# Kernel optimization log

Hardware: AMD Instinct MI355X
Metric: run time of the kernel (lower is better)

The kernel has to match this reference:

```python
import jax, jax.numpy as jnp
import numpy as np

D, H, W = 40, 32, 88
BEV_H, BEV_W = 125, 125
X_MIN, X_MAX, DX = -50.0, 50.0, 0.8
Y_MIN, Y_MAX, DY = -50.0, 50.0, 0.8
Z_MIN, DZ = -10.0, 20.0


def _voxel_indices():
    """Replicates frustum creation + get_geometry + index computation.
    Returns (flat_idx, valid) each of shape (D, H, W). Faithful to the
    original's sequential in-place max() semantics."""
    # depth_grid = arange(1, 41, 1) + 1  -> 2..41
    depth = jnp.arange(1.0, 41.0, 1.0) + 1.0            # (D,)
    xs = jnp.linspace(0.0, W - 1.0, W)                  # (W,)
    ys = jnp.linspace(0.0, H - 1.0, H)                  # (H,)
    d = depth[:, None, None]                            # (D,1,1)
    xd = jnp.broadcast_to(xs[None, None, :] * d, (D, H, W))  # x*depth
    yd = jnp.broadcast_to(ys[None, :, None] * d, (D, H, W))  # y*depth
    zd = jnp.broadcast_to(d, (D, H, W))                       # depth
    # first points_d.max(): over columns (xd, yd, zd)
    max1 = jnp.maximum(xd.max(), jnp.maximum(yd.max(), zd.max()))
    gx = xd / max1 * (X_MAX - X_MIN) + X_MIN
    # second points_d.max(): column 0 was overwritten in-place by gx
    max2 = jnp.maximum(gx.max(), jnp.maximum(yd.max(), zd.max()))
    gy = yd / max2 * (Y_MAX - Y_MIN) + Y_MIN
    gz = zd
    # voxelize (torch .long() truncates; all values here are >= 0)
    ix = ((gx - X_MIN) / DX).astype(jnp.int32)
    iy = ((gy - Y_MIN) / DY).astype(jnp.int32)
    iz = ((gz - Z_MIN) / DZ).astype(jnp.int32)
    valid = (ix >= 0) & (ix < BEV_W) & (iy >= 0) & (iy < BEV_H) & (iz >= 0)
    flat_idx = jnp.where(valid, iy * BEV_W + ix, 0)
    return flat_idx, valid


def setup_inputs() -> dict:
    key = jax.random.key(0)
    k1, k2, k3, k4, k5 = jax.random.split(key, 5)
    B, N, C = 1, 6, 128
    return {
        "img_feat": jax.random.normal(k1, (B, N, C, H, W), dtype=jnp.float32),
        "depth_logits": jax.random.normal(k2, (B, N, D, H, W), dtype=jnp.float32),
        "rots": jax.random.normal(k3, (B, N, 3, 3), dtype=jnp.float32),
        "trans": jax.random.normal(k4, (B, N, 3), dtype=jnp.float32),
        "intrins": jax.random.normal(k5, (B, N, 3, 3), dtype=jnp.float32),
    }


def reference(img_feat, depth_logits, rots, trans, intrins):
    B, N, C, h, w = img_feat.shape
    depth_probs = jax.nn.softmax(depth_logits, axis=2)         # (B,N,D,H,W)
    # depth-weighted outer product: (B,N,D,H,W,C)
    feats = jnp.einsum('bnchw,bndhw->bndhwc', img_feat, depth_probs)
    flat_feats = feats.reshape(-1, C)                          # (B*N*D*H*W, C)
    flat_idx, valid = _voxel_indices()                         # (D,H,W)
    idx = jnp.broadcast_to(flat_idx[None, None], (B, N, D, h, w)).reshape(-1)
    msk = jnp.broadcast_to(valid[None, None], (B, N, D, h, w)).reshape(-1)
    flat_feats = jnp.where(msk[:, None], flat_feats, 0.0)
    bev = jax.ops.segment_sum(flat_feats, idx, num_segments=BEV_H * BEV_W)
    bev = bev.reshape(BEV_H, BEV_W, C)
    return jnp.transpose(bev, (2, 0, 1))[None]                 # (1, C, 125, 125)
```

## Files before the change

kernel.cpp:

```cpp
#include <hip/hip_runtime.h>


constexpr int D = 40, H = 32, W = 88, HW = H * W;
constexpr int C = 128, NCAM = 6;
constexpr int BEV = 125, NBINS = BEV * BEV;
constexpr int NCOLS = NCAM * HW;
constexpr int LISTCAP = 192;

typedef __attribute__((ext_vector_type(8))) unsigned short us8;
typedef __attribute__((ext_vector_type(4))) float f4;

__device__ __forceinline__ unsigned short f2bf(float x) {
    unsigned u = __float_as_uint(x);
    return (unsigned short)((u + 0x7FFF + ((u >> 16) & 1)) >> 16);
}
__device__ __forceinline__ float b2f(unsigned short u) {
    return __uint_as_float(((unsigned)u) << 16);
}

struct Tabs { short XP[D][126]; short YP[D][126]; };
constexpr Tabs make_tabs() {
    Tabs t{};
    for (int d = 0; d < D; ++d) {
        int dep = d + 2;
        int cntx[126] = {};
        for (int w = 0; w < W; ++w) {
            float gx = (float)(w * dep) / 3567.0f * 100.0f - 50.0f;
            int ix = (int)((gx + 50.0f) / 0.8f);
            if (ix < 125) cntx[ix]++;
        }
        t.XP[d][0] = 0;
        for (int X = 0; X < 125; ++X) t.XP[d][X + 1] = (short)(t.XP[d][X] + cntx[X]);
        int cnty[126] = {};
        for (int h = 0; h < H; ++h) {
            float gy = (float)(h * dep) / 1271.0f * 100.0f - 50.0f;
            int iy = (int)((gy + 50.0f) / 0.8f);
            if (iy < 125) cnty[iy]++;
        }
        t.YP[d][0] = 0;
        for (int Y = 0; Y < 125; ++Y) t.YP[d][Y + 1] = (short)(t.YP[d][Y] + cnty[Y]);
    }
    return t;
}
__device__ const Tabs g_tab = make_tabs();

struct SegTable { unsigned a[4096]; unsigned b[4096]; int n; };

constexpr SegTable make_segs() {
    SegTable S{};
    Tabs t = make_tabs();
    int ns = 0;
    for (int iy = 0; iy < 125; ++iy) {
        int cnt[125] = {};
        for (int d = 0; d < D; ++d) {
            int yc = t.YP[d][iy + 1] - t.YP[d][iy];
            if (yc == 0) continue;
            for (int X = 0; X < 125; ++X)
                cnt[X] += (t.XP[d][X + 1] - t.XP[d][X]) * yc;
        }
        int X = 0;
        while (X < 125) {
            if (cnt[X] > 176) {
                int d0 = 0;
                while (d0 < D) {
                    int run = 0, d1 = d0;
                    while (d1 < D) {
                        int piece = (t.XP[d1][X + 1] - t.XP[d1][X]) *
                                    (t.YP[d1][iy + 1] - t.YP[d1][iy]);
                        if (d1 > d0 && run + piece > 128) break;
                        run += piece; ++d1;
                    }
                    if (run > 0) {
                        S.a[ns] = ((unsigned)iy << 16) | ((unsigned)X << 8) | (unsigned)(X + 1);
                        S.b[ns] = (1u << 31) | ((unsigned)d0 << 25) | ((unsigned)d1 << 19) | (unsigned)run;
                        ++ns;
                    }
                    d0 = d1;
                }
                ++X;
            } else {
                int X0 = X, run = 0;
                while (X < 125 && (X - X0) < 16 && cnt[X] <= 176 &&
                       (X == X0 || run + cnt[X] <= 128)) {
                    run += cnt[X]; ++X;
                }
                if (run > 0) {
                    S.a[ns] = ((unsigned)iy << 16) | ((unsigned)X0 << 8) | (unsigned)X;
                    S.b[ns] = ((unsigned)0 << 25) | ((unsigned)D << 19) | (unsigned)run;
                    ++ns;
                }
            }
        }
    }
    S.n = ns;
    return S;
}
constexpr SegTable g_raw = make_segs();

constexpr SegTable reorder_segs() {
    SegTable R{};
    int pos = 0;
    for (int i = 0; i < g_raw.n; ++i)
        if ((int)(g_raw.b[i] & 0x7FFFF) >= 120) { R.a[pos] = g_raw.a[i]; R.b[pos] = g_raw.b[i]; ++pos; }
    for (int i = 0; i < g_raw.n; ++i)
        if ((int)(g_raw.b[i] & 0x7FFFF) <  120) { R.a[pos] = g_raw.a[i]; R.b[pos] = g_raw.b[i]; ++pos; }
    R.n = pos;
    return R;
}
constexpr SegTable g_ct = reorder_segs();
constexpr int NSEG = g_ct.n;
static_assert(NSEG > 0 && NSEG <= 4096, "seg table overflow");
__device__ const SegTable g_segs = g_ct;

constexpr int PACK_BLOCKS = (C / 8) * (HW / 32);
constexpr int SMAX_BLOCKS = NCOLS / 256;
constexpr int ZERO_TOTAL  = C * NBINS / 4;
constexpr int ZERO_BLOCKS = (ZERO_TOTAL + 1023) / 1024;
constexpr int MEGA_BLOCKS = PACK_BLOCKS + SMAX_BLOCKS + ZERO_BLOCKS;

__global__ void __launch_bounds__(256) mega_kernel(
        const float* __restrict__ feat,
        const float* __restrict__ logits,
        float* __restrict__ probs_t,
        unsigned short* __restrict__ feat_p,
        float* __restrict__ out) {
    __shared__ __align__(16) float tile[NCAM * 8 * 37];
    int b = blockIdx.x, t = threadIdx.x;

    if (b < PACK_BLOCKS) {
        int c0  = (b / 88) * 8;
        int hw0 = (b % 88) * 32;
        int cq = t >> 5, hwL = t & 31;
#pragma unroll
        for (int n = 0; n < NCAM; ++n)
            tile[(n * 8 + cq) * 37 + hwL] =
                feat[((size_t)(n * C + c0 + cq)) * HW + hw0 + hwL];
        __syncthreads();
        int hl = t >> 3, cL = t & 7;
        us8 v;
#pragma unroll
        for (int n = 0; n < NCAM; ++n)
            v[n] = f2bf(tile[(n * 8 + cL) * 37 + hl]);
        v[6] = 0; v[7] = 0;
        *(us8*)(feat_p + ((size_t)(hw0 + hl) * C + (c0 + cL)) * 8) = v;

    } else if (b < PACK_BLOCKS + SMAX_BLOCKS) {
        int col = (b - PACK_BLOCKS) * 256 + t;
        int n  = col / HW;
        int hw = col - n * HW;
        const float* src = logits + ((size_t)n * D) * HW + hw;
        float v[D];
        float m = -3.402823466e+38f;
#pragma unroll
        for (int d = 0; d < D; ++d) {
            v[d] = src[(size_t)d * HW];
            m = fmaxf(m, v[d]);
        }
        float s = 0.f;
#pragma unroll
        for (int d = 0; d < D; ++d) { v[d] = expf(v[d] - m); s += v[d]; }
        float inv = 1.0f / s;
#pragma unroll
        for (int d = 0; d < D; ++d)
            probs_t[(size_t)((d << 12) | hw) * 8 + n] = v[d] * inv;

    } else {
        int base = (b - PACK_BLOCKS - SMAX_BLOCKS) * 1024;
#pragma unroll
        for (int k = 0; k < 4; ++k) {
            int i = base + k * 256 + t;
            if (i < ZERO_TOTAL) ((f4*)out)[i] = f4{0.f, 0.f, 0.f, 0.f};
        }
    }
}

__global__ void __launch_bounds__(128, 4) gather_kernel(
        const unsigned short* __restrict__ feat_p,
        const float* __restrict__ probs_t,
        float* __restrict__ out) {
    __shared__ float T[2][16][66];
    __shared__ unsigned list[LISTCAP];
    int slot  = blockIdx.x >> 1;
    int chalf = blockIdx.x & 1;
    unsigned da = g_segs.a[slot], db = g_segs.b[slot];
    int iy = da >> 16, X0 = (da >> 8) & 0xFF, X1 = da & 0xFF;
    int width = X1 - X0;
    bool split = (db >> 31) != 0;
    int d0 = (db >> 25) & 0x3F, d1 = (db >> 19) & 0x3F;
    int P  = (int)(db & 0x7FFFF);
    int t = threadIdx.x;

    if (t < 64) {
        int d = d0 + t;
        if (d < d1) {
            int off = 0;
            for (int dd = d0; dd < d; ++dd)
                off += (g_tab.YP[dd][iy + 1] - g_tab.YP[dd][iy]) *
                       (g_tab.XP[dd][X1] - g_tab.XP[dd][X0]);
            int hb = g_tab.YP[d][iy], he = g_tab.YP[d][iy + 1];
            int p = off;
            for (int bl = 0; bl < width; ++bl) {
                int wb = g_tab.XP[d][X0 + bl], we = g_tab.XP[d][X0 + bl + 1];
                for (int h = hb; h < he; ++h)
                    for (int w = wb; w < we; ++w)
                        list[p++] = ((unsigned)bl << 18) | ((unsigned)d << 12)
                                  | (unsigned)(h * W + w);
            }
        }
    } else {
        float* Tf = &T[0][0][0];
        for (int i = t - 64; i < 2 * 16 * 66; i += 64) Tf[i] = 0.f;
    }
    __syncthreads();

    int lane = t & 63, dg = t >> 6;
    int c = chalf * 64 + lane;
    float* Tp = &T[dg][0][0];

    int npts = (P - dg + 1) >> 1;
    float racc = 0.f;
    int rbl = -1;

#define FETCH(I, BUF, P_)                                                     \
    { pk##BUF[I] = (unsigned)__shfl(myent, (P_));                             \
      fv##BUF[I] = *(const us8*)(feat_p +                                     \
                    (((size_t)(pk##BUF[I] & 0xFFFu) * C + (unsigned)c) * 8)); \
      const float* pp_ = probs_t + ((size_t)(pk##BUF[I] & 0x3FFFFu) << 3);    \
      pa##BUF[I] = *(const f4*)pp_; pb##BUF[I] = *(const f4*)(pp_ + 4); }
#define CONSUME(I, BUF)                                                       \
    { float s_ = pa##BUF[I].x * b2f(fv##BUF[I][0]) + pa##BUF[I].y * b2f(fv##BUF[I][1]) \
               + pa##BUF[I].z * b2f(fv##BUF[I][2]) + pa##BUF[I].w * b2f(fv##BUF[I][3]) \
               + pb##BUF[I].x * b2f(fv##BUF[I][4]) + pb##BUF[I].y * b2f(fv##BUF[I][5]);\
      int bl_ = (int)(pk##BUF[I] >> 18);                                      \
      if (bl_ != rbl) { if (rbl >= 0) Tp[rbl * 66 + lane] += racc;            \
                        rbl = bl_; racc = s_; }                               \
      else racc += s_; }

    int li0 = min(dg + 2 * lane, LISTCAP - 1);
    int myent_next = (int)list[li0];
    for (int kb = 0; kb < npts; kb += 64) {
        int myent = myent_next;
        if (kb + 64 < npts) {
            int li = min(dg + 2 * (kb + 64 + lane), LISTCAP - 1);
            myent_next = (int)list[li];
        }
        int win = min(64, npts - kb);
        unsigned pkA[3], pkB[3]; us8 fvA[3], fvB[3];
        f4 paA[3], pbA[3], paB[3], pbB[3];
#pragma unroll
        for (int i = 0; i < 3; ++i) if (i < win) FETCH(i, A, i);
        for (int j = 0; j < win; j += 6) {
#pragma unroll
            for (int i = 0; i < 3; ++i) { int p = j + 3 + i;
                if (p < win) FETCH(i, B, p); }
#pragma unroll
            for (int i = 0; i < 3; ++i) { int p = j + i;
                if (p < win) CONSUME(i, A); }
#pragma unroll
            for (int i = 0; i < 3; ++i) { int p = j + 6 + i;
                if (p < win) FETCH(i, A, p); }
#pragma unroll
            for (int i = 0; i < 3; ++i) { int p = j + 3 + i;
                if (p < win) CONSUME(i, B); }
        }
    }
    if (rbl >= 0) Tp[rbl * 66 + lane] += racc;
    __syncthreads();
#undef FETCH
#undef CONSUME

    int binbase = iy * BEV + X0;
#pragma unroll
    for (int it = 0; it < 8; ++it) {
        int bl = t & 15, cc = it * 8 + (t >> 4);
        if (bl < width) {
            float v = T[0][bl][cc] + T[1][bl][cc];
            float* dst = &out[(size_t)(chalf * 64 + cc) * NBINS + binbase + bl];
            if (split) atomicAdd(dst, v);
            else       *dst = v;
        }
    }
}

extern "C" void kernel_launch(void* const* d_in, const int* in_sizes, int n_in,
                              void* d_out, int out_size, void* d_ws, size_t ws_size,
                              hipStream_t stream) {
    const float* img_feat     = (const float*)d_in[0];
    const float* depth_logits = (const float*)d_in[1];
    float* out = (float*)d_out;

    char* p = (char*)d_ws;
    float*          probs_t = (float*)p;          p += (size_t)D * 4096 * 8 * 4;
    unsigned short* feat_p  = (unsigned short*)p; p += (size_t)HW * C * 8 * 2;

    mega_kernel<<<MEGA_BLOCKS, 256, 0, stream>>>(
        img_feat, depth_logits, probs_t, feat_p, out);
    gather_kernel<<<NSEG * 2, 128, 0, stream>>>(feat_p, probs_t, out);
}
```

Measured before the change: 124.6 us.

## Prebuild per-segment gather lists in mega kernel with flush flags

Moves construction of each segment's point list out of the gather kernel's shared-memory prologue and into extra blocks of the mega kernel, which write a global list per segment, split by depth group and padded to groups of four. Each entry carries a flush bit marking where a bin run ends. The gather kernel reads entries wave-uniformly as uint4 plus readfirstlane and runs a branch-light double-buffered loop, replacing the per-block serial list build and the shuffle-based indexing. In exchange it adds global list traffic, padding entries that do useless gathers, and more builder blocks in the first kernel.

```diff
diff --git a/kernel.cpp b/kernel.cpp
--- a/kernel.cpp
+++ b/kernel.cpp
@@ -5,10 +5,10 @@
 constexpr int C = 128, NCAM = 6;
 constexpr int BEV = 125, NBINS = BEV * BEV;
 constexpr int NCOLS = NCAM * HW;
-constexpr int LISTCAP = 192;
 
 typedef __attribute__((ext_vector_type(8))) unsigned short us8;
 typedef __attribute__((ext_vector_type(4))) float f4;
+typedef __attribute__((ext_vector_type(2))) float f2;
 
 __device__ __forceinline__ unsigned short f2bf(float x) {
     unsigned u = __float_as_uint(x);
@@ -42,21 +42,21 @@
     }
     return t;
 }
-__device__ const Tabs g_tab = make_tabs();
+constexpr Tabs g_tabs = make_tabs();
+__device__ const Tabs g_tab = g_tabs;
 
 struct SegTable { unsigned a[4096]; unsigned b[4096]; int n; };
 
 constexpr SegTable make_segs() {
     SegTable S{};
-    Tabs t = make_tabs();
     int ns = 0;
     for (int iy = 0; iy < 125; ++iy) {
         int cnt[125] = {};
         for (int d = 0; d < D; ++d) {
-            int yc = t.YP[d][iy + 1] - t.YP[d][iy];
+            int yc = g_tabs.YP[d][iy + 1] - g_tabs.YP[d][iy];
             if (yc == 0) continue;
             for (int X = 0; X < 125; ++X)
-                cnt[X] += (t.XP[d][X + 1] - t.XP[d][X]) * yc;
+                cnt[X] += (g_tabs.XP[d][X + 1] - g_tabs.XP[d][X]) * yc;
         }
         int X = 0;
         while (X < 125) {
@@ -65,8 +65,8 @@
                 while (d0 < D) {
                     int run = 0, d1 = d0;
                     while (d1 < D) {
-                        int piece = (t.XP[d1][X + 1] - t.XP[d1][X]) *
-                                    (t.YP[d1][iy + 1] - t.YP[d1][iy]);
+                        int piece = (g_tabs.XP[d1][X + 1] - g_tabs.XP[d1][X]) *
+                                    (g_tabs.YP[d1][iy + 1] - g_tabs.YP[d1][iy]);
                         if (d1 > d0 && run + piece > 128) break;
                         run += piece; ++d1;
                     }
@@ -112,11 +112,35 @@
 static_assert(NSEG > 0 && NSEG <= 4096, "seg table overflow");
 __device__ const SegTable g_segs = g_ct;
 
-constexpr int PACK_BLOCKS = (C / 8) * (HW / 32);
-constexpr int SMAX_BLOCKS = NCOLS / 256;
-constexpr int ZERO_TOTAL  = C * NBINS / 4;
-constexpr int ZERO_BLOCKS = (ZERO_TOTAL + 1023) / 1024;
-constexpr int MEGA_BLOCKS = PACK_BLOCKS + SMAX_BLOCKS + ZERO_BLOCKS;
+struct Meta { unsigned m[4096]; int ne; };
+constexpr Meta make_meta() {
+    Meta M{};
+    int pos = 0;
+    for (int i = 0; i < NSEG; ++i) {
+        int cnt = (int)(g_ct.b[i] & 0x7FFFF);
+        int ng = (((cnt + 1) >> 1) + 3) >> 2;
+        M.m[i] = (g_ct.b[i] & 0x80000000u) | ((unsigned)pos << 10) | (unsigned)ng;
+        pos += 2 * ng * 4;
+    }
+    M.ne = pos;
+    return M;
+}
+constexpr Meta g_mt = make_meta();
+constexpr int NE_TOT = g_mt.ne;
+static_assert(NE_TOT < (1 << 21), "start field overflow");
+__device__ const unsigned g_meta[4096] = {};
+struct MetaArr { unsigned m[4096]; };
+constexpr MetaArr make_meta_arr() { MetaArr A{}; for (int i = 0; i < 4096; ++i) A.m[i] = g_mt.m[i]; return A; }
+__device__ const MetaArr g_metaD = make_meta_arr();
+
+__device__ __align__(16) unsigned g_glist[NE_TOT + 64];
+
+constexpr int PACK_BLOCKS  = (C / 8) * (HW / 32);
+constexpr int SMAX_BLOCKS  = NCOLS / 256;
+constexpr int BUILD_BLOCKS = (NSEG + 255) / 256;
+constexpr int ZERO_TOTAL   = C * NBINS / 4;
+constexpr int ZERO_BLOCKS  = (ZERO_TOTAL + 1023) / 1024;
+constexpr int MEGA_BLOCKS  = PACK_BLOCKS + SMAX_BLOCKS + BUILD_BLOCKS + ZERO_BLOCKS;
 
 __global__ void __launch_bounds__(256) mega_kernel(
         const float* __restrict__ feat,
@@ -164,8 +188,47 @@
         for (int d = 0; d < D; ++d)
             probs_t[(size_t)((d << 12) | hw) * 8 + n] = v[d] * inv;
 
+    } else if (b < PACK_BLOCKS + SMAX_BLOCKS + BUILD_BLOCKS) {
+        int slot = (b - PACK_BLOCKS - SMAX_BLOCKS) * 256 + t;
+        if (slot < NSEG) {
+            unsigned da = g_segs.a[slot], db = g_segs.b[slot];
+            int iy = (int)(da >> 16), X0 = (int)((da >> 8) & 0xFF), X1 = (int)(da & 0xFF);
+            int d0 = (int)((db >> 25) & 0x3F), d1 = (int)((db >> 19) & 0x3F);
+            unsigned mb = g_metaD.m[slot];
+            int ng4 = (int)(mb & 0x3FFu) * 4;
+            unsigned* gl = g_glist + ((mb >> 10) & 0x1FFFFFu);
+            unsigned pend0 = 0, pend1 = 0;
+            int j = 0;
+            for (int bl = 0; bl < X1 - X0; ++bl)
+                for (int d = d0; d < d1; ++d) {
+                    int hb = g_tab.YP[d][iy], he = g_tab.YP[d][iy + 1];
+                    int wb = g_tab.XP[d][X0 + bl], we = g_tab.XP[d][X0 + bl + 1];
+                    for (int h = hb; h < he; ++h)
+                        for (int w = wb; w < we; ++w) {
+                            unsigned v = ((unsigned)bl << 19) | ((unsigned)d << 12)
+                                       | (unsigned)(h * W + w);
+                            if (j >= 2) {
+                                unsigned u = (j & 1) ? pend1 : pend0;
+                                if (((u >> 19) & 31u) != (unsigned)bl) u |= 0x80000000u;
+                                int jj = j - 2;
+                                gl[(jj & 1) * ng4 + (jj >> 1)] = u;
+                            }
+                            if (j & 1) pend1 = v; else pend0 = v;
+                            ++j;
+                        }
+                }
+            for (int jj = (j >= 2 ? j - 2 : 0); jj < j; ++jj)
+                gl[(jj & 1) * ng4 + (jj >> 1)] =
+                    ((jj & 1) ? pend1 : pend0) | 0x80000000u;
+            for (int dgj = 0; dgj < 2; ++dgj) {
+                int cnt = (j + 1 - dgj) >> 1;
+                for (int k = cnt; k < ng4; ++k)
+                    gl[dgj * ng4 + k] = (16u << 19) | 0x80000000u;
+            }
+        }
+
     } else {
-        int base = (b - PACK_BLOCKS - SMAX_BLOCKS) * 1024;
+        int base = (b - PACK_BLOCKS - SMAX_BLOCKS - BUILD_BLOCKS) * 1024;
 #pragma unroll
         for (int k = 0; k < 4; ++k) {
             int i = base + k * 256 + t;
@@ -178,96 +241,68 @@
         const unsigned short* __restrict__ feat_p,
         const float* __restrict__ probs_t,
         float* __restrict__ out) {
-    __shared__ float T[2][16][66];
-    __shared__ unsigned list[LISTCAP];
-    int slot  = blockIdx.x >> 1;
-    int chalf = blockIdx.x & 1;
-    unsigned da = g_segs.a[slot], db = g_segs.b[slot];
-    int iy = da >> 16, X0 = (da >> 8) & 0xFF, X1 = da & 0xFF;
+    __shared__ __align__(16) float T[2][17][66];
+    int t = threadIdx.x;
+    int slot = blockIdx.x >> 1, chalf = blockIdx.x & 1;
+    unsigned da = g_segs.a[slot], mb = g_metaD.m[slot];
+    int iy = (int)(da >> 16), X0 = (int)((da >> 8) & 0xFF), X1 = (int)(da & 0xFF);
     int width = X1 - X0;
-    bool split = (db >> 31) != 0;
-    int d0 = (db >> 25) & 0x3F, d1 = (db >> 19) & 0x3F;
-    int P  = (int)(db & 0x7FFFF);
-    int t = threadIdx.x;
-
-    if (t < 64) {
-        int d = d0 + t;
-        if (d < d1) {
-            int off = 0;
-            for (int dd = d0; dd < d; ++dd)
-                off += (g_tab.YP[dd][iy + 1] - g_tab.YP[dd][iy]) *
-                       (g_tab.XP[dd][X1] - g_tab.XP[dd][X0]);
-            int hb = g_tab.YP[d][iy], he = g_tab.YP[d][iy + 1];
-            int p = off;
-            for (int bl = 0; bl < width; ++bl) {
-                int wb = g_tab.XP[d][X0 + bl], we = g_tab.XP[d][X0 + bl + 1];
-                for (int h = hb; h < he; ++h)
-                    for (int w = wb; w < we; ++w)
-                        list[p++] = ((unsigned)bl << 18) | ((unsigned)d << 12)
-                                  | (unsigned)(h * W + w);
-            }
-        }
-    } else {
-        float* Tf = &T[0][0][0];
-        for (int i = t - 64; i < 2 * 16 * 66; i += 64) Tf[i] = 0.f;
-    }
+    bool split = (mb >> 31) != 0;
+    int ng = (int)(mb & 0x3FFu);
+    unsigned start = (mb >> 10) & 0x1FFFFFu;
+    int dg = __builtin_amdgcn_readfirstlane((int)(threadIdx.x >> 6));
+    int lane = t & 63;
+    int c = chalf * 64 + lane;
+
+    { float* Tf = &T[0][0][0];
+      for (int i = t; i < 2 * 17 * 66; i += 128) Tf[i] = 0.f; }
     __syncthreads();
 
-    int lane = t & 63, dg = t >> 6;
-    int c = chalf * 64 + lane;
+    const unsigned* ep = g_glist + (start + (unsigned)(dg * ng * 4));
+    const unsigned short* fbase = feat_p + (size_t)c * 8;
     float* Tp = &T[dg][0][0];
-
-    int npts = (P - dg + 1) >> 1;
     float racc = 0.f;
-    int rbl = -1;
-
-#define FETCH(I, BUF, P_)                                                     \
-    { pk##BUF[I] = (unsigned)__shfl(myent, (P_));                             \
-      fv##BUF[I] = *(const us8*)(feat_p +                                     \
-                    (((size_t)(pk##BUF[I] & 0xFFFu) * C + (unsigned)c) * 8)); \
-      const float* pp_ = probs_t + ((size_t)(pk##BUF[I] & 0x3FFFFu) << 3);    \
-      pa##BUF[I] = *(const f4*)pp_; pb##BUF[I] = *(const f4*)(pp_ + 4); }
-#define CONSUME(I, BUF)                                                       \
-    { float s_ = pa##BUF[I].x * b2f(fv##BUF[I][0]) + pa##BUF[I].y * b2f(fv##BUF[I][1]) \
-               + pa##BUF[I].z * b2f(fv##BUF[I][2]) + pa##BUF[I].w * b2f(fv##BUF[I][3]) \
-               + pb##BUF[I].x * b2f(fv##BUF[I][4]) + pb##BUF[I].y * b2f(fv##BUF[I][5]);\
-      int bl_ = (int)(pk##BUF[I] >> 18);                                      \
-      if (bl_ != rbl) { if (rbl >= 0) Tp[rbl * 66 + lane] += racc;            \
-                        rbl = bl_; racc = s_; }                               \
-      else racc += s_; }
-
-    int li0 = min(dg + 2 * lane, LISTCAP - 1);
-    int myent_next = (int)list[li0];
-    for (int kb = 0; kb < npts; kb += 64) {
-        int myent = myent_next;
-        if (kb + 64 < npts) {
-            int li = min(dg + 2 * (kb + 64 + lane), LISTCAP - 1);
-            myent_next = (int)list[li];
-        }
-        int win = min(64, npts - kb);
-        unsigned pkA[3], pkB[3]; us8 fvA[3], fvB[3];
-        f4 paA[3], pbA[3], paB[3], pbB[3];
-#pragma unroll
-        for (int i = 0; i < 3; ++i) if (i < win) FETCH(i, A, i);
-        for (int j = 0; j < win; j += 6) {
-#pragma unroll
-            for (int i = 0; i < 3; ++i) { int p = j + 3 + i;
-                if (p < win) FETCH(i, B, p); }
-#pragma unroll
-            for (int i = 0; i < 3; ++i) { int p = j + i;
-                if (p < win) CONSUME(i, A); }
-#pragma unroll
-            for (int i = 0; i < 3; ++i) { int p = j + 6 + i;
-                if (p < win) FETCH(i, A, p); }
-#pragma unroll
-            for (int i = 0; i < 3; ++i) { int p = j + 3 + i;
-                if (p < win) CONSUME(i, B); }
-        }
-    }
-    if (rbl >= 0) Tp[rbl * 66 + lane] += racc;
+
+#define LOADE(E, g_) { uint4 ee_ = *(const uint4*)(ep + 4 * (g_));            \
+    E[0] = (unsigned)__builtin_amdgcn_readfirstlane((int)ee_.x);              \
+    E[1] = (unsigned)__builtin_amdgcn_readfirstlane((int)ee_.y);              \
+    E[2] = (unsigned)__builtin_amdgcn_readfirstlane((int)ee_.z);              \
+    E[3] = (unsigned)__builtin_amdgcn_readfirstlane((int)ee_.w); }
+#define ISSUE(S, E) _Pragma("unroll") for (int i_ = 0; i_ < 4; ++i_) {        \
+    fv##S[i_] = *(const us8*)(fbase + ((size_t)(E[i_] & 0xFFFu) << 10));      \
+    const float* pp_ = probs_t + ((size_t)(E[i_] & 0x3FFFFu) << 3);           \
+    pa##S[i_] = *(const f4*)pp_; pb##S[i_] = *(const f2*)(pp_ + 4); }
+#define CONS(S, E) _Pragma("unroll") for (int i_ = 0; i_ < 4; ++i_) {         \
+    racc += pa##S[i_].x * b2f(fv##S[i_][0]) + pa##S[i_].y * b2f(fv##S[i_][1]) \
+          + pa##S[i_].z * b2f(fv##S[i_][2]) + pa##S[i_].w * b2f(fv##S[i_][3]) \
+          + pb##S[i_].x * b2f(fv##S[i_][4]) + pb##S[i_].y * b2f(fv##S[i_][5]);\
+    if (E[i_] & 0x80000000u) {                                                \
+        Tp[((E[i_] >> 19) & 31u) * 66 + (unsigned)lane] += racc; racc = 0.f; } }
+
+    unsigned EA[4], EB[4], ET[4];
+    us8 fvA[4], fvB[4];
+    f4 paA[4], paB[4];
+    f2 pbA[4], pbB[4];
+    LOADE(EA, 0); LOADE(EB, 1);
+    ISSUE(A, EA);
+    int g = 0;
+    for (; g + 2 <= ng; g += 2) {
+        ISSUE(B, EB);
+        LOADE(ET, g + 2);
+        CONS(A, EA);
+        if (g + 2 < ng) {
+            ISSUE(A, ET);
+#pragma unroll
+            for (int q = 0; q < 4; ++q) EA[q] = ET[q];
+        }
+        CONS(B, EB);
+        LOADE(EB, g + 3);
+    }
+    if (g < ng) CONS(A, EA);
+#undef LOADE
+#undef ISSUE
+#undef CONS
     __syncthreads();
-#undef FETCH
-#undef CONSUME
 
     int binbase = iy * BEV + X0;
 #pragma unroll
```

After: 367.5 us. 195% more time.
